# Kernel optimization log

Hardware: AMD Instinct MI355X
Metric: run time of the kernel (lower is better)

## Reference

```python
import jax, jax.numpy as jnp
import numpy as np

MODULE_OUTPUT_CLIP_VAL = 100.0
ACTION_MEAN_CLIP_VAL = 1000.0
ACTION_STD = 0.05
SURPRISE_SCALE_FACTOR = 1.0
SM_BASELINE = 1.0  # registered buffer, init 1.0


def setup_inputs() -> dict:
    key = jax.random.key(0)
    ks = jax.random.split(key, 9)
    D, H = 16384, 4096

    def lin(k, fan_in, shape):
        bound = 1.0 / np.sqrt(fan_in)
        return jax.random.uniform(k, shape, jnp.float32, -bound, bound)

    return {
        "ct": jax.random.normal(ks[0], (D,), jnp.float32),
        "W1": lin(ks[1], D, (D, H)),
        "b1": lin(ks[2], D, (H,)),
        "W2": lin(ks[3], H, (H, H)),
        "b2": lin(ks[4], H, (H,)),
        "W3": lin(ks[5], H, (H, D)),
        "b3": lin(ks[6], H, (D,)),
        "qm": jax.random.normal(ks[7], (D,), jnp.float32) * 0.01,
        "noise": jax.random.normal(ks[8], (D,), jnp.float32),
        "k_sparse": 512,
    }


def reference(ct, W1, b1, W2, b2, W3, b3, qm, noise, k_sparse):
    ct_d = jax.lax.stop_gradient(ct)  # ct.detach() in both predict and gate

    # predict(): 3-layer MLP with ReLU, clamped
    h = jax.nn.relu(ct_d @ W1 + b1)
    h = jax.nn.relu(h @ W2 + b2)
    vm = jnp.clip(h @ W3 + b3, -MODULE_OUTPUT_CLIP_VAL, MODULE_OUTPUT_CLIP_VAL)

    # generate_write_vector()
    tau_g = 1.0
    gate = jax.nn.sigmoid(qm * ct_d / tau_g)
    # current_surprise_for_alpha == sm_baseline -> diff is exactly 0
    surprise_diff = SM_BASELINE - SM_BASELINE
    influence = jnp.clip(1.0 + 1.0 * jnp.tanh(SURPRISE_SCALE_FACTOR * surprise_diff), 0.1, 10.0)
    action_mean = jnp.clip(influence * (gate * vm), -ACTION_MEAN_CLIP_VAL, ACTION_MEAN_CLIP_VAL)

    # Normal(mean, std).sample() is non-differentiable -> stop_gradient
    sample = jax.lax.stop_gradient(action_mean + ACTION_STD * noise)
    log_prob = jnp.sum(
        -0.5 * ((sample - action_mean) / ACTION_STD) ** 2
        - jnp.log(jnp.float32(ACTION_STD))
        - 0.5 * jnp.log(jnp.float32(2.0 * np.pi))
    )

    # sparsify: keep top-k by magnitude, zeros elsewhere (dense representation of sparse COO)
    _, idx = jax.lax.top_k(jnp.abs(sample), k_sparse)
    write_vec = jnp.zeros_like(sample).at[idx].set(sample[idx])
    return write_vec, log_prob
```

## Files before the change

kernel.cpp:

```cpp
#include <hip/hip_runtime.h>
#include <math.h>


constexpr int D = 16384;
constexpr int H = 4096;

__device__ __forceinline__ void stage16(const float* g, const float* l) {
    __builtin_amdgcn_global_load_lds(
        (const __attribute__((address_space(1))) unsigned int*)g,
        (__attribute__((address_space(3))) unsigned int*)l,
        16, 0, 0);
}

__device__ __forceinline__ double wredsum(double v) {
    #pragma unroll
    for (int o = 32; o > 0; o >>= 1) v += __shfl_down(v, o, 64);
    return v;
}

template<int KC, bool FRED>
__global__ __launch_bounds__(256) void k_mv(
    const float* __restrict__ W, int N, int K,
    const float* __restrict__ xf,
    const double* __restrict__ xpart,
    int Gprev,
    const float* __restrict__ bias,
    double* __restrict__ ypart)
{
    constexpr int NWC = (KC + 63) / 64;
    __shared__ float wbuf[4][2][8][256];
    __shared__ double xv[KC];
    __shared__ double xred[256];
    __shared__ int cidx[KC];
    __shared__ int wtot[NWC > 0 ? NWC : 1];
    __shared__ int s_nt;

    const int t = threadIdx.x, lane = t & 63, w = t >> 6;
    const int k0 = blockIdx.y * KC;

    if constexpr (!FRED) {
        if (t < KC) { xv[t] = (double)xf[k0 + t]; cidx[t] = t; }
        if (t == 0) s_nt = KC / 8;
    } else {
        constexpr int NS = 256 / KC;
        {
            const int kl = t & (KC - 1), sl = t / KC;
            double s = 0.0;
            for (int g = sl; g < Gprev; g += NS)
                s += xpart[(size_t)g * K + k0 + kl];
            xred[t] = s;
        }
        __syncthreads();
        double x = 0.0; bool pred = false;
        if (t < KC) {
            double tot = (double)bias[k0 + t];
            #pragma unroll
            for (int s2 = 0; s2 < NS; ++s2) tot += xred[s2 * KC + t];
            x = tot > 0.0 ? tot : 0.0;
            pred = x > 0.0;
        }
        const unsigned long long mask = __ballot(pred);
        const int rank = __popcll(mask & ((1ull << lane) - 1ull));
        const int tot  = __popcll(mask);
        if (t < KC && lane == 0) wtot[t >> 6] = tot;
        __syncthreads();
        int woffs = 0;
        #pragma unroll
        for (int ww = 0; ww < NWC; ++ww)
            if (ww < (t >> 6)) woffs += wtot[ww];
        if (pred) { cidx[woffs + rank] = t; xv[woffs + rank] = x; }
        int m = 0;
        #pragma unroll
        for (int ww = 0; ww < NWC; ++ww) m += wtot[ww];
        const int m8 = (m + 7) & ~7;
        __syncthreads();
        if (t >= m && t < m8) { cidx[t] = 0; xv[t] = 0.0; }
        if (t == 0) s_nt = m8 / 8;
    }
    __syncthreads();
    const int nt = s_nt;

    const int cbase = blockIdx.x * 1024 + w * 256;
    const float* Wg = W + (size_t)k0 * N + cbase + lane * 4;
    float* b0 = &wbuf[w][0][0][0];
    float* b1 = &wbuf[w][1][0][0];
    double a0 = 0, a1 = 0, a2 = 0, a3 = 0;

    if (nt > 0) {
        #pragma unroll
        for (int r = 0; r < 8; ++r)
            stage16(Wg + (size_t)cidx[r] * N, b0 + r * 256);

        for (int tt = 0; tt < nt; ++tt) {
            if (tt + 1 < nt) {
                const int j = (tt + 1) * 8;
                #pragma unroll
                for (int r = 0; r < 8; ++r)
                    stage16(Wg + (size_t)cidx[j + r] * N, b1 + r * 256);
                asm volatile("s_waitcnt vmcnt(8)" ::: "memory");
            } else {
                asm volatile("s_waitcnt vmcnt(0)" ::: "memory");
            }
            #pragma unroll
            for (int r = 0; r < 8; ++r) {
                const float4 wv = *reinterpret_cast<const float4*>(b0 + r * 256 + lane * 4);
                const double x = xv[tt * 8 + r];
                a0 += x * (double)wv.x; a1 += x * (double)wv.y;
                a2 += x * (double)wv.z; a3 += x * (double)wv.w;
            }
            float* tmp = b0; b0 = b1; b1 = tmp;
        }
    }

    double* yp = ypart + (size_t)blockIdx.y * N + cbase + lane * 4;
    *reinterpret_cast<double2*>(yp + 0) = make_double2(a0, a1);
    *reinterpret_cast<double2*>(yp + 2) = make_double2(a2, a3);
}

__global__ __launch_bounds__(256) void k_finalize(
    const double* __restrict__ p3, int G,
    const float* __restrict__ b3,
    const float* __restrict__ qm,
    const float* __restrict__ ct,
    const float* __restrict__ noise,
    float* __restrict__ samp,
    double* __restrict__ lpp)
{
    const int i = blockIdx.x * 256 + threadIdx.x;
    double s0 = 0, s1 = 0;
    #pragma unroll 4
    for (int g = 0; g + 1 < G; g += 2) {
        s0 += p3[(size_t)g * D + i];
        s1 += p3[(size_t)(g + 1) * D + i];
    }
    double vm = (double)b3[i] + s0 + s1;
    vm = vm > 100.0 ? 100.0 : (vm < -100.0 ? -100.0 : vm);
    const double z = (double)qm[i] * (double)ct[i];
    const double g = 1.0 / (1.0 + exp(-z));
    double am = g * vm;
    am = am > 1000.0 ? 1000.0 : (am < -1000.0 ? -1000.0 : am);
    const float amf = (float)am;
    const float sp = amf + 0.05f * noise[i];
    samp[i] = sp;
    const float df = (sp - amf) / 0.05f;
    double term = (double)df * (double)df;
    term = wredsum(term);
    __shared__ double red[4];
    const int lane = threadIdx.x & 63, wid = threadIdx.x >> 6;
    if (lane == 0) red[wid] = term;
    __syncthreads();
    if (threadIdx.x == 0) lpp[blockIdx.x] = red[0] + red[1] + red[2] + red[3];
}

#define TPK 1024
__global__ __launch_bounds__(TPK) void k_topk(
    const float* __restrict__ samp,
    const int* __restrict__ kptr,
    const double* __restrict__ lpp, int GLP,
    float* __restrict__ out)
{
    __shared__ unsigned int u[16384];
    __shared__ int whist[16][257];
    __shared__ int hist[256];
    __shared__ int sfx[256];
    __shared__ int wsum[16];
    __shared__ int wcnt[4];
    __shared__ unsigned int s_prefix;
    __shared__ int s_kk;

    const int t = threadIdx.x;
    const int lane = t & 63, wid = t >> 6;

    for (int i = t; i < D; i += TPK)
        u[i] = __float_as_uint(samp[i]) & 0x7fffffffu;
    __syncthreads();

    const int k = *kptr;
    unsigned int prefix = 0;
    int kk = k;
    for (int pass = 0; pass < 4; ++pass) {
        const int shift = 24 - 8 * pass;
        const unsigned int dm = pass ? (0xffffffffu << (32 - 8 * pass)) : 0u;
        for (int i = t; i < 16 * 257; i += TPK) (&whist[0][0])[i] = 0;
        __syncthreads();
        for (int i = t; i < D; i += TPK) {
            const unsigned int v = u[i];
            if ((v & dm) == prefix)
                atomicAdd(&whist[wid][(v >> shift) & 0xff], 1);
        }
        __syncthreads();
        if (t < 256) {
            int s = 0;
            #pragma unroll
            for (int w = 0; w < 16; ++w) s += whist[w][t];
            hist[t] = s;
            sfx[t] = s;
        }
        __syncthreads();
        #pragma unroll
        for (int off = 1; off < 256; off <<= 1) {
            int add = 0;
            if (t < 256 && t + off < 256) add = sfx[t + off];
            __syncthreads();
            if (t < 256) sfx[t] += add;
            __syncthreads();
        }
        const bool cond = (t < 256) && (sfx[t] >= kk);
        const unsigned long long m = __ballot(cond);
        if (lane == 0 && wid < 4) wcnt[wid] = __popcll(m);
        __syncthreads();
        if (t == 0) {
            const int bs = wcnt[0] + wcnt[1] + wcnt[2] + wcnt[3] - 1;
            s_kk = kk - (sfx[bs] - hist[bs]);
            s_prefix = prefix | ((unsigned int)bs << shift);
        }
        __syncthreads();
        prefix = s_prefix;
        kk = s_kk;
        __syncthreads();
    }
    const unsigned int vstar = prefix;
    const int need = kk;

    constexpr int PER = D / TPK;
    const int base = t * PER;
    float vals[PER];
    unsigned int keys[PER];
    int cnt = 0;
    #pragma unroll
    for (int j = 0; j < PER; ++j) {
        const float f = samp[base + j];
        vals[j] = f;
        keys[j] = __float_as_uint(f) & 0x7fffffffu;
        cnt += (keys[j] == vstar) ? 1 : 0;
    }
    int inc = cnt;
    #pragma unroll
    for (int o = 1; o < 64; o <<= 1) {
        const int n = __shfl_up(inc, o, 64);
        if (lane >= o) inc += n;
    }
    if (lane == 63) wsum[wid] = inc;
    __syncthreads();
    int woff = 0;
    for (int w = 0; w < wid; ++w) woff += wsum[w];
    int offset = woff + inc - cnt;
    #pragma unroll
    for (int j = 0; j < PER; ++j) {
        float o2 = 0.0f;
        if (keys[j] > vstar) {
            o2 = vals[j];
        } else if (keys[j] == vstar) {
            if (offset < need) o2 = vals[j];
            offset++;
        }
        out[base + j] = o2;
    }

    if (wid == 0) {
        double s = 0;
        for (int g = lane; g < GLP; g += 64) s += lpp[g];
        s = wredsum(s);
        if (lane == 0) {
            const double c = -log(0.05) - 0.5 * log(2.0 * 3.14159265358979323846);
            out[D] = (float)(-0.5 * s + (double)D * c);
        }
    }
}

extern "C" void kernel_launch(void* const* d_in, const int* in_sizes, int n_in,
                              void* d_out, int out_size, void* d_ws, size_t ws_size,
                              hipStream_t stream) {
    const float* ct    = (const float*)d_in[0];
    const float* W1    = (const float*)d_in[1];
    const float* b1    = (const float*)d_in[2];
    const float* W2    = (const float*)d_in[3];
    const float* b2    = (const float*)d_in[4];
    const float* W3    = (const float*)d_in[5];
    const float* b3    = (const float*)d_in[6];
    const float* qm    = (const float*)d_in[7];
    const float* noise = (const float*)d_in[8];
    const int*   kp    = (const int*)d_in[9];

    constexpr int KC1 = 128, KC2 = 32, KC3 = 128;
    constexpr int G1 = D / KC1;
    constexpr int G2 = H / KC2;
    constexpr int G3 = H / KC3;
    constexpr int GLP = D / 256;

    double* p1   = (double*)d_ws;
    double* p2   = p1 + (size_t)G1 * H;
    double* p3   = p2 + (size_t)G2 * H;
    float*  samp = (float*)(p3 + (size_t)G3 * D);
    double* lpp  = (double*)(samp + D);

    k_mv<KC1, false><<<dim3(H / 1024, G1), 256, 0, stream>>>(
        W1, H, D, ct, nullptr, 0, nullptr, p1);
    k_mv<KC2, true><<<dim3(H / 1024, G2), 256, 0, stream>>>(
        W2, H, H, nullptr, p1, G1, b1, p2);
    k_mv<KC3, true><<<dim3(D / 1024, G3), 256, 0, stream>>>(
        W3, D, H, nullptr, p2, G2, b2, p3);
    k_finalize<<<dim3(D / 256), 256, 0, stream>>>(
        p3, G3, b3, qm, ct, noise, samp, lpp);
    k_topk<<<dim3(1), TPK, 0, stream>>>(samp, kp, lpp, GLP, (float*)d_out);
}
```

Before: 148.0 us.

## Accumulate split-K GEMV partials with fp64 atomics instead of partial buffers

Each split-K block now adds its partial dot products directly into a single output vector with double-precision atomic adds, replacing per-group partial arrays that the next stage had to read and reduce. This removes the partial-buffer writes and the reduction reads at the start of each following layer and in the finalize kernel. In exchange it adds a memset of the accumulators, atomic contention on each output element, and summation order that is no longer deterministic.

```diff
diff --git a/kernel.cpp b/kernel.cpp
--- a/kernel.cpp
+++ b/kernel.cpp
@@ -20,17 +20,15 @@
 
 template<int KC, bool FRED>
 __global__ __launch_bounds__(256) void k_mv(
-    const float* __restrict__ W, int N, int K,
+    const float* __restrict__ W, int N,
     const float* __restrict__ xf,
-    const double* __restrict__ xpart,
-    int Gprev,
+    const double* __restrict__ yprev,
     const float* __restrict__ bias,
-    double* __restrict__ ypart)
+    double* __restrict__ yout)
 {
     constexpr int NWC = (KC + 63) / 64;
     __shared__ float wbuf[4][2][8][256];
     __shared__ double xv[KC];
-    __shared__ double xred[256];
     __shared__ int cidx[KC];
     __shared__ int wtot[NWC > 0 ? NWC : 1];
     __shared__ int s_nt;
@@ -42,21 +40,10 @@
         if (t < KC) { xv[t] = (double)xf[k0 + t]; cidx[t] = t; }
         if (t == 0) s_nt = KC / 8;
     } else {
-        constexpr int NS = 256 / KC;
-        {
-            const int kl = t & (KC - 1), sl = t / KC;
-            double s = 0.0;
-            for (int g = sl; g < Gprev; g += NS)
-                s += xpart[(size_t)g * K + k0 + kl];
-            xred[t] = s;
-        }
-        __syncthreads();
         double x = 0.0; bool pred = false;
         if (t < KC) {
-            double tot = (double)bias[k0 + t];
-            #pragma unroll
-            for (int s2 = 0; s2 < NS; ++s2) tot += xred[s2 * KC + t];
-            x = tot > 0.0 ? tot : 0.0;
+            const double v = yprev[k0 + t] + (double)bias[k0 + t];
+            x = v > 0.0 ? v : 0.0;
             pred = x > 0.0;
         }
         const unsigned long long mask = __ballot(pred);
@@ -112,13 +99,15 @@
         }
     }
 
-    double* yp = ypart + (size_t)blockIdx.y * N + cbase + lane * 4;
-    *reinterpret_cast<double2*>(yp + 0) = make_double2(a0, a1);
-    *reinterpret_cast<double2*>(yp + 2) = make_double2(a2, a3);
+    const int c = cbase + lane * 4;
+    unsafeAtomicAdd(&yout[c + 0], a0);
+    unsafeAtomicAdd(&yout[c + 1], a1);
+    unsafeAtomicAdd(&yout[c + 2], a2);
+    unsafeAtomicAdd(&yout[c + 3], a3);
 }
 
 __global__ __launch_bounds__(256) void k_finalize(
-    const double* __restrict__ p3, int G,
+    const double* __restrict__ y3,
     const float* __restrict__ b3,
     const float* __restrict__ qm,
     const float* __restrict__ ct,
@@ -127,13 +116,7 @@
     double* __restrict__ lpp)
 {
     const int i = blockIdx.x * 256 + threadIdx.x;
-    double s0 = 0, s1 = 0;
-    #pragma unroll 4
-    for (int g = 0; g + 1 < G; g += 2) {
-        s0 += p3[(size_t)g * D + i];
-        s1 += p3[(size_t)(g + 1) * D + i];
-    }
-    double vm = (double)b3[i] + s0 + s1;
+    double vm = y3[i] + (double)b3[i];
     vm = vm > 100.0 ? 100.0 : (vm < -100.0 ? -100.0 : vm);
     const double z = (double)qm[i] * (double)ct[i];
     const double g = 1.0 / (1.0 + exp(-z));
@@ -284,23 +267,24 @@
 
     constexpr int KC1 = 128, KC2 = 32, KC3 = 128;
     constexpr int G1 = D / KC1;
-    constexpr int G2 = H / KC2;
-    constexpr int G3 = H / KC3;
     constexpr int GLP = D / 256;
-
-    double* p1   = (double*)d_ws;
-    double* p2   = p1 + (size_t)G1 * H;
-    double* p3   = p2 + (size_t)G2 * H;
-    float*  samp = (float*)(p3 + (size_t)G3 * D);
+    (void)G1;
+
+    double* y1   = (double*)d_ws;
+    double* y2   = y1 + H;
+    double* y3   = y2 + H;
+    float*  samp = (float*)(y3 + D);
     double* lpp  = (double*)(samp + D);
 
-    k_mv<KC1, false><<<dim3(H / 1024, G1), 256, 0, stream>>>(
-        W1, H, D, ct, nullptr, 0, nullptr, p1);
-    k_mv<KC2, true><<<dim3(H / 1024, G2), 256, 0, stream>>>(
-        W2, H, H, nullptr, p1, G1, b1, p2);
-    k_mv<KC3, true><<<dim3(D / 1024, G3), 256, 0, stream>>>(
-        W3, D, H, nullptr, p2, G2, b2, p3);
+    hipMemsetAsync(d_ws, 0, (size_t)(2 * H + D) * 8, stream);
+
+    k_mv<KC1, false><<<dim3(H / 1024, D / KC1), 256, 0, stream>>>(
+        W1, H, ct, nullptr, nullptr, y1);
+    k_mv<KC2, true><<<dim3(H / 1024, H / KC2), 256, 0, stream>>>(
+        W2, H, nullptr, y1, b1, y2);
+    k_mv<KC3, true><<<dim3(D / 1024, H / KC3), 256, 0, stream>>>(
+        W3, D, nullptr, y2, b2, y3);
     k_finalize<<<dim3(D / 256), 256, 0, stream>>>(
-        p3, G3, b3, qm, ct, noise, samp, lpp);
+        y3, b3, qm, ct, noise, samp, lpp);
     k_topk<<<dim3(1), TPK, 0, stream>>>(samp, kp, lpp, GLP, (float*)d_out);
 }
```

After: 163.1 us. 10.1% more time.
